# Kernel optimization log

Measured on AMD Instinct MI355X. Metric: run time of the kernel, lower is better.

The kernel has to match this reference:

```python
import jax, jax.numpy as jnp
import numpy as np

EMB = 128     # embedding_size
HEADS = 4     # n_heads
LAYERS = 2    # n_layers
T = 10        # number of graphs / timesteps (== window_size)
N = 20000     # nodes per graph
E = 320000    # edges per graph
B = 4096      # clf_nodes
WIN = 10      # window_size
NEG_SLOPE = 0.2


def setup_inputs() -> dict:
    key = jax.random.key(0)
    ks = jax.random.split(key, 26)
    p = lambda k, shape: 0.05 * jax.random.normal(k, shape, jnp.float32)
    inp = {
        "embeddings": jax.random.normal(ks[0], (T, N, EMB), jnp.float32),
        "edges": jax.random.randint(ks[1], (T, 2, E), 0, N),
        "node_type": jax.random.randint(ks[2], (T, N), 0, 4),
        "edge_type": jax.random.randint(ks[3], (T, E), 0, 4),
        "clf_neighbors": jax.random.randint(ks[4], (B,), 0, N),
        "clf_nodes": jax.random.randint(ks[5], (B,), 0, N),
        # branch 1 GAT stacks: lin weight [L, H*C, D], attention vecs [L, H, C], bias [L, H*C]
        "gat_W1": p(ks[6], (LAYERS, HEADS * EMB, EMB)),
        "gat_as1": p(ks[7], (LAYERS, HEADS, EMB)),
        "gat_ad1": p(ks[8], (LAYERS, HEADS, EMB)),
        "gat_b1": p(ks[9], (LAYERS, HEADS * EMB)),
        "lin_W1": p(ks[10], (LAYERS, EMB, HEADS * EMB)),
        "lin_b1": p(ks[11], (LAYERS, EMB)),
        # branch 2
        "gat_W2": p(ks[12], (LAYERS, HEADS * EMB, EMB)),
        "gat_as2": p(ks[13], (LAYERS, HEADS, EMB)),
        "gat_ad2": p(ks[14], (LAYERS, HEADS, EMB)),
        "gat_b2": p(ks[15], (LAYERS, HEADS * EMB)),
        "lin_W2": p(ks[16], (LAYERS, EMB, HEADS * EMB)),
        "lin_b2": p(ks[17], (LAYERS, EMB)),
        # head MLP (fc1 consumes flattened [window * 2*D])
        "fc1_W": p(ks[18], (EMB, 2 * EMB * WIN)),
        "fc1_b": p(ks[19], (EMB,)),
        "fc2_W": p(ks[20], (2, EMB)),
        "fc2_b": p(ks[21], (2,)),
    }
    return inp


def _gat(x, src, dst, W, a_s, a_d, b):
    """PyG-style GATConv (concat=True, self-loops already in src/dst, eval mode)."""
    n = x.shape[0]
    h = (x @ W.T).reshape(n, HEADS, EMB)                       # [N,H,C]
    logits = jax.nn.leaky_relu((h * a_s).sum(-1)[src] + (h * a_d).sum(-1)[dst], NEG_SLOPE)  # [Etot,H]
    logits = logits - jax.ops.segment_max(logits, dst, num_segments=n)[dst]
    ex = jnp.exp(logits)
    alpha = ex / jax.ops.segment_sum(ex, dst, num_segments=n)[dst]  # segment softmax over targets
    out = jax.ops.segment_sum(alpha[:, :, None] * h[src], dst, num_segments=n)  # [N,H,C]
    return out.reshape(n, HEADS * EMB) + b


def _branch(embeddings, edges, gW, gas, gad, gb, lW, lb):
    loops = jnp.arange(N)

    def step(carry, inputs):
        x, edge = inputs
        src = jnp.concatenate([edge[0], loops])  # add self loops (PyG default)
        dst = jnp.concatenate([edge[1], loops])
        for i in range(LAYERS):
            x = _gat(x, src, dst, gW[i], gas[i], gad[i], gb[i])
            x = jax.nn.relu(x @ lW[i].T + lb[i])
        return carry, x

    _, outs = jax.lax.scan(step, 0, (embeddings, edges))
    return outs  # [T,N,EMB]


def reference(embeddings, edges, node_type, edge_type, clf_neighbors, clf_nodes,
              gat_W1, gat_as1, gat_ad1, gat_b1, lin_W1, lin_b1,
              gat_W2, gat_as2, gat_ad2, gat_b2, lin_W2, lin_b2,
              fc1_W, fc1_b, fc2_W, fc2_b):
    o1 = _branch(embeddings, edges, gat_W1, gat_as1, gat_ad1, gat_b1, lin_W1, lin_b1)
    o2 = _branch(embeddings, edges, gat_W2, gat_as2, gat_ad2, gat_b2, lin_W2, lin_b2)
    # original prepends each graph's output -> reversed timestep order
    e1 = o1[::-1][:, clf_nodes].transpose(1, 0, 2)  # [B,T,EMB]
    e2 = o2[::-1][:, clf_nodes].transpose(1, 0, 2)
    temp = jnp.concatenate([e1, e2], axis=2)        # [B,T,2*EMB]
    # slen == window_size -> skip buffer is fully filled by temp
    flat = temp.reshape(temp.shape[0], WIN * 2 * EMB)
    h = jax.nn.relu(flat @ fc1_W.T + fc1_b)
    return jax.nn.relu(h @ fc2_W.T + fc2_b)        # [B,2]
```

## Files before the change

kernel.cpp:

```cpp
#include <hip/hip_runtime.h>
#include <cstdint>

#define NNODES 20000
#define NEDGES 320000
#define ETOT   340000
#define TSTEPS 10
#define BCLF   4096
#define EMB    128
#define HC     512
#define NEG_SLOPE 0.2f

#define NSB    64
#define SBSPAN 313
#define PCAP   6912
#define ECHUNK 2048
#define NCHUNKS ((NEDGES + ECHUNK - 1) / ECHUNK)
#define NSCHUNK ((NNODES + 255) / 256)
#define STAGECAP 7424

typedef _Float16 half_t;
typedef __attribute__((ext_vector_type(8))) _Float16 half8;
typedef __attribute__((ext_vector_type(4))) float floatx4;

__global__ void cvt_split_kernel(const float* __restrict__ in,
                                 half_t* __restrict__ hi, half_t* __restrict__ lo, long n4) {
    long i = (long)blockIdx.x * 256 + threadIdx.x;
    if (i >= n4) return;
    float4 v = *(const float4*)&in[i * 4];
    half_t h[4], l[4];
    h[0] = (half_t)v.x; l[0] = (half_t)(v.x - (float)h[0]);
    h[1] = (half_t)v.y; l[1] = (half_t)(v.y - (float)h[1]);
    h[2] = (half_t)v.z; l[2] = (half_t)(v.z - (float)h[2]);
    h[3] = (half_t)v.w; l[3] = (half_t)(v.w - (float)h[3]);
    *(unsigned long long*)&hi[i * 4] = *(unsigned long long*)h;
    *(unsigned long long*)&lo[i * 4] = *(unsigned long long*)l;
}

__global__ __launch_bounds__(256) void part64_kernel(const int* __restrict__ edges,
                                                     int* __restrict__ bcnt,
                                                     int* __restrict__ pairs) {
    int g = blockIdx.y;
    int c = blockIdx.x;
    __shared__ int hist[NSB], gbase[NSB], cur[NSB];
    if (threadIdx.x < NSB) hist[threadIdx.x] = 0;
    __syncthreads();
    const int* srcp = edges + (long)g * 2 * NEDGES;
    const int* dstp = srcp + NEDGES;
    int e0 = c * ECHUNK + threadIdx.x;
    int s[8], d[8], sb[8];
#pragma unroll
    for (int i = 0; i < 8; i++) {
        int e = e0 + i * 256;
        if (e < NEDGES) {
            s[i] = srcp[e];
            d[i] = dstp[e];
            sb[i] = (int)((unsigned)d[i] / (unsigned)SBSPAN);
            atomicAdd(&hist[sb[i]], 1);
        } else sb[i] = -1;
    }
    __syncthreads();
    if (threadIdx.x < NSB) {
        int h = hist[threadIdx.x];
        gbase[threadIdx.x] = h ? atomicAdd(&bcnt[g * NSB + threadIdx.x], h) : 0;
        cur[threadIdx.x] = 0;
    }
    __syncthreads();
#pragma unroll
    for (int i = 0; i < 8; i++) {
        if (sb[i] >= 0) {
            int pos = gbase[sb[i]] + atomicAdd(&cur[sb[i]], 1);
            int v = s[i] | ((d[i] - sb[i] * SBSPAN) << 15);
            pairs[((long)(g * NSB + sb[i])) * PCAP + pos] = v;
        }
    }
}

__global__ __launch_bounds__(256) void count_sb_kernel(const int* __restrict__ pairs,
                                                       const int* __restrict__ bcnt,
                                                       int* __restrict__ counts) {
    int g = blockIdx.x >> 6, sb = blockIdx.x & 63;
    __shared__ int hist[SBSPAN];
    for (int i = threadIdx.x; i < SBSPAN; i += 256) hist[i] = 0;
    __syncthreads();
    int n0 = sb * SBSPAN;
    int cnt = bcnt[g * NSB + sb];
    const int* p = pairs + (long)(g * NSB + sb) * PCAP;
    for (int k = threadIdx.x; k < cnt; k += 256)
        atomicAdd(&hist[p[k] >> 15], 1);
    __syncthreads();
    int nn = min(SBSPAN, NNODES - n0);
    for (int i = threadIdx.x; i < nn; i += 256)
        counts[g * NNODES + n0 + i] = hist[i];
}

__global__ void scanA_kernel(const int* __restrict__ counts, int* __restrict__ bsum) {
    int g = blockIdx.x / NSCHUNK, ch = blockIdx.x % NSCHUNK;
    int i = ch * 256 + threadIdx.x;
    int v = (i < NNODES) ? counts[g * NNODES + i] + 1 : 0;
    for (int off = 32; off; off >>= 1) v += __shfl_down(v, off);
    __shared__ int ws[4];
    if ((threadIdx.x & 63) == 0) ws[threadIdx.x >> 6] = v;
    __syncthreads();
    if (threadIdx.x == 0) bsum[blockIdx.x] = ws[0] + ws[1] + ws[2] + ws[3];
}

__global__ void scanB_kernel(const int* __restrict__ bsum, int* __restrict__ boff,
                             int* __restrict__ rowptr) {
    int g = blockIdx.x;
    int tid = threadIdx.x;
    int v = (tid < NSCHUNK) ? bsum[g * NSCHUNK + tid] : 0;
    __shared__ int buf[128];
    buf[tid] = v;
    __syncthreads();
    for (int off = 1; off < 128; off <<= 1) {
        int t = (tid >= off) ? buf[tid - off] : 0;
        __syncthreads();
        buf[tid] += t;
        __syncthreads();
    }
    if (tid < NSCHUNK) boff[g * NSCHUNK + tid] = buf[tid] - v;
    if (tid == 127) rowptr[g * (NNODES + 1) + NNODES] = buf[127];
}

__global__ void scanC_kernel(const int* __restrict__ counts, const int* __restrict__ boff,
                             int* __restrict__ rowptr) {
    int g = blockIdx.x / NSCHUNK, ch = blockIdx.x % NSCHUNK;
    int tid = threadIdx.x;
    int i = ch * 256 + tid;
    int v = (i < NNODES) ? counts[g * NNODES + i] + 1 : 0;
    __shared__ int buf[256];
    buf[tid] = v;
    __syncthreads();
    for (int off = 1; off < 256; off <<= 1) {
        int t = (tid >= off) ? buf[tid - off] : 0;
        __syncthreads();
        buf[tid] += t;
        __syncthreads();
    }
    int excl = boff[blockIdx.x] + buf[tid] - v;
    if (i < NNODES) rowptr[g * (NNODES + 1) + i] = excl;
}

__global__ __launch_bounds__(256) void fill_sb_kernel(const int* __restrict__ pairs,
                                                      const int* __restrict__ bcnt,
                                                      const int* __restrict__ rowptr,
                                                      int* __restrict__ csr_src) {
    int g = blockIdx.x >> 6, sb = blockIdx.x & 63;
    __shared__ int cur[SBSPAN];
    __shared__ int stage[STAGECAP];
    int n0 = sb * SBSPAN;
    int nn = min(SBSPAN, NNODES - n0);
    const int* rp = rowptr + g * (NNODES + 1);
    int base = rp[n0];
    int span = rp[n0 + nn] - base;
    for (int i = threadIdx.x; i < nn; i += 256) {
        int rb = rp[n0 + i] - base;
        stage[rb] = n0 + i;
        cur[i] = rb + 1;
    }
    __syncthreads();
    int cnt = bcnt[g * NSB + sb];
    const int* p = pairs + (long)(g * NSB + sb) * PCAP;
    for (int k = threadIdx.x; k < cnt; k += 256) {
        int v = p[k];
        int pos = atomicAdd(&cur[v >> 15], 1);
        stage[pos] = v & 0x7fff;
    }
    __syncthreads();
    int* dst = csr_src + (long)g * ETOT + base;
    for (int k = threadIdx.x; k < span; k += 256) dst[k] = stage[k];
}

__global__ void prep_was_kernel(const float* __restrict__ W1, const float* __restrict__ W2,
                                const float* __restrict__ as1, const float* __restrict__ as2,
                                const float* __restrict__ ad1, const float* __restrict__ ad2,
                                float* __restrict__ was, float* __restrict__ wad) {
    int b = blockIdx.x;
    int l = b >> 3, z = (b >> 2) & 1, h = b & 3;
    int k = threadIdx.x;
    const float* W  = z ? W2 : W1;
    const float* av = z ? as2 : as1;
    const float* dv = z ? ad2 : ad1;
    float s = 0.f, d = 0.f;
    for (int c = 0; c < 128; c++) {
        float w = W[(long)l * HC * EMB + (h * 128 + c) * 128 + k];
        s = fmaf(w, av[(l * 4 + h) * 128 + c], s);
        d = fmaf(w, dv[(l * 4 + h) * 128 + c], d);
    }
    long idx = ((l * 2 + z) * 4 + h) * 128 + k;
    was[idx] = s;
    wad[idx] = d;
}

__global__ void pack_ws_kernel(const float* __restrict__ wasb, const float* __restrict__ wadb,
                               half_t* __restrict__ WS0h, half_t* __restrict__ WS0l,
                               half_t* __restrict__ WS1h, half_t* __restrict__ WS1l) {
    int b = blockIdx.x;
    int k = threadIdx.x;
    if (b < 16) {
        int z = b >> 3, d = (b >> 2) & 1, h = b & 3;
        const float* src = d ? wadb : wasb;
        float v = src[((long)z * 4 + h) * 128 + k];
        half_t hi = (half_t)v;
        WS0h[b * 128 + k] = hi;
        WS0l[b * 128 + k] = (half_t)(v - (float)hi);
    } else {
        int b2 = b - 16;
        int z = b2 >> 4, r = b2 & 15;
        float v = 0.f;
        if (r < 8) {
            int d = r >> 2, h = r & 3;
            const float* src = d ? wadb : wasb;
            v = src[((long)(2 + z) * 4 + h) * 128 + k];
        }
        half_t hi = (half_t)v;
        WS1h[(z * 16 + r) * 128 + k] = hi;
        WS1l[(z * 16 + r) * 128 + k] = (half_t)(v - (float)hi);
    }
}

__global__ void prep_M_kernel(const float* __restrict__ gW1, const float* __restrict__ gW2,
                              const float* __restrict__ lW1, const float* __restrict__ lW2,
                              half_t* __restrict__ Mh, half_t* __restrict__ Ml) {
    int k = blockIdx.x;
    int inst = blockIdx.y;
    int l = inst >> 1, z = inst & 1;
    int c = threadIdx.x;
    const float* gW = (z ? gW2 : gW1) + (long)l * HC * EMB;
    const float* lW = (z ? lW2 : lW1) + (long)l * EMB * HC;
    float acc[4] = {0.f, 0.f, 0.f, 0.f};
    for (int cp = 0; cp < 128; cp++) {
#pragma unroll
        for (int h = 0; h < 4; h++) {
            float lw = lW[(long)k * 512 + h * 128 + cp];
            float gw = gW[(long)(h * 128 + cp) * 128 + c];
            acc[h] = fmaf(lw, gw, acc[h]);
        }
    }
#pragma unroll
    for (int h = 0; h < 4; h++) {
        long o = ((long)inst * 128 + k) * 512 + h * 128 + c;
        half_t hi = (half_t)acc[h];
        Mh[o] = hi;
        Ml[o] = (half_t)(acc[h] - (float)hi);
    }
}

__global__ void prep_cb_kernel(const float* __restrict__ lW1, const float* __restrict__ lW2,
                               const float* __restrict__ gb1_, const float* __restrict__ gb2_,
                               const float* __restrict__ lb1_, const float* __restrict__ lb2_,
                               float* __restrict__ cb) {
    int inst = blockIdx.x;
    int l = inst >> 1, z = inst & 1;
    int k = threadIdx.x;
    const float* lW = (z ? lW2 : lW1) + (long)l * EMB * HC;
    const float* gb = (z ? gb2_ : gb1_) + l * HC;
    const float* lb = (z ? lb2_ : lb1_) + l * EMB;
    float a = lb[k];
    for (int j = 0; j < 512; j++) a = fmaf(lW[(long)k * 512 + j], gb[j], a);
    cb[inst * 128 + k] = a;
}

__global__ __launch_bounds__(256) void scores_b(
    const half_t* __restrict__ Ahb, const half_t* __restrict__ Alb, long aInst,
    const half_t* __restrict__ WShb, const half_t* __restrict__ WSlb, long wInst, int wMask,
    float* __restrict__ outb, long oInst, int M, int OS, int CMAX) {
    int iy = blockIdx.y;
    const half_t* Ah = Ahb + (long)iy * aInst;
    const half_t* Al = Alb + (long)iy * aInst;
    const half_t* WSh = WShb + (long)(iy & wMask) * wInst;
    const half_t* WSl = WSlb + (long)(iy & wMask) * wInst;
    float* out = outb + (long)iy * oInst;
    __shared__ half_t Bh[16 * 128];
    __shared__ half_t Bl[16 * 128];
    int tid = threadIdx.x;
    *(half8*)&Bh[tid * 8] = *(const half8*)&WSh[tid * 8];
    *(half8*)&Bl[tid * 8] = *(const half8*)&WSl[tid * 8];
    __syncthreads();
    int wave = tid >> 6, lane = tid & 63;
    int l16 = lane & 15, chunk = lane >> 4;
    int r0 = blockIdx.x * 64 + wave * 16;
    int rowc = r0 + l16; if (rowc > M - 1) rowc = M - 1;
    floatx4 acc = (floatx4)0.f;
#pragma unroll
    for (int ko = 0; ko < 128; ko += 32) {
        half8 ah = *(const half8*)&Ah[(long)rowc * 128 + ko + chunk * 8];
        half8 al = *(const half8*)&Al[(long)rowc * 128 + ko + chunk * 8];
        half8 bh = *(const half8*)&Bh[l16 * 128 + ko + chunk * 8];
        half8 bl = *(const half8*)&Bl[l16 * 128 + ko + chunk * 8];
        acc = __builtin_amdgcn_mfma_f32_16x16x32_f16(ah, bh, acc, 0, 0, 0);
        acc = __builtin_amdgcn_mfma_f32_16x16x32_f16(ah, bl, acc, 0, 0, 0);
        acc = __builtin_amdgcn_mfma_f32_16x16x32_f16(al, bh, acc, 0, 0, 0);
    }
#pragma unroll
    for (int reg = 0; reg < 4; reg++) {
        int rr = r0 + chunk * 4 + reg;
        if (rr < M && l16 < CMAX) out[(long)rr * OS + l16] = acc[reg];
    }
}

template <bool SX>
__global__ __launch_bounds__(256) void agg2_kernel(
    const half_t* __restrict__ X0b, const half_t* __restrict__ X1b, long xsT,
    const float* __restrict__ sAb, const float* __restrict__ sBb, int stsh, long ssT,
    const int* __restrict__ rowptr, const int* __restrict__ csr_src,
    half_t* __restrict__ Yh, half_t* __restrict__ Yl, int t0) {
    int tz = blockIdx.y, t = t0 + tz;
    int n = blockIdx.x * 4 + (threadIdx.x >> 6);
    int lane = threadIdx.x & 63;
    int h = lane >> 4, cg = lane & 15;
    const int* rp = rowptr + t * (NNODES + 1);
    int beg = rp[n], end = rp[n + 1];
    const int* cs = csr_src + (long)t * ETOT;
    const half_t* X0 = X0b + (long)tz * xsT;
    const half_t* X1 = SX ? X0 : (X1b + (long)tz * xsT);
    const float* sA = sAb + (long)tz * ssT;
    const float* sB = sBb + (long)tz * ssT;
    float sd0 = sA[((long)n << stsh) + 4 + h];
    float sd1 = sB[((long)n << stsh) + 4 + h];
    float acc0[8], acc1[8];
#pragma unroll
    for (int c = 0; c < 8; c++) { acc0[c] = 0.f; acc1[c] = 0.f; }
    float den0 = 0.f, den1 = 0.f;

    auto proc2 = [&](int s0, int s1) {
        float va0 = sA[((long)s0 << stsh) + h];
        float vb0 = sB[((long)s0 << stsh) + h];
        float va1 = sA[((long)s1 << stsh) + h];
        float vb1 = sB[((long)s1 << stsh) + h];
        half8 xa0 = *(const half8*)&X0[(long)s0 * 128 + cg * 8];
        half8 xa1 = *(const half8*)&X0[(long)s1 * 128 + cg * 8];
        half8 xb0, xb1;
        if (!SX) {
            xb0 = *(const half8*)&X1[(long)s0 * 128 + cg * 8];
            xb1 = *(const half8*)&X1[(long)s1 * 128 + cg * 8];
        }
        float La0 = va0 + sd0, Lb0 = vb0 + sd1;
        float La1 = va1 + sd0, Lb1 = vb1 + sd1;
        float wa0 = __expf(fmaxf(La0, NEG_SLOPE * La0));
        float wb0 = __expf(fmaxf(Lb0, NEG_SLOPE * Lb0));
        float wa1 = __expf(fmaxf(La1, NEG_SLOPE * La1));
        float wb1 = __expf(fmaxf(Lb1, NEG_SLOPE * Lb1));
        den0 += wa0 + wa1;
        den1 += wb0 + wb1;
#pragma unroll
        for (int c = 0; c < 8; c++) {
            float a = acc0[c];
            a = fmaf(wa0, (float)xa0[c], a);
            a = fmaf(wa1, (float)xa1[c], a);
            acc0[c] = a;
            float b = acc1[c];
            b = fmaf(wb0, (float)(SX ? xa0[c] : xb0[c]), b);
            b = fmaf(wb1, (float)(SX ? xa1[c] : xb1[c]), b);
            acc1[c] = b;
        }
    };

    int j = beg;
    if (end - beg >= 4) {
        int a0 = cs[j], a1 = cs[j + 1];
        while (j + 4 <= end) {
            int b0 = cs[j + 2], b1 = cs[j + 3];
            proc2(a0, a1);
            a0 = b0; a1 = b1;
            j += 2;
        }
        proc2(a0, a1);
        j += 2;
    }
    for (; j < end; j++) {
        int src = cs[j];
        float va = sA[((long)src << stsh) + h];
        float vb = sB[((long)src << stsh) + h];
        half8 xa = *(const half8*)&X0[(long)src * 128 + cg * 8];
        half8 xb;
        if (!SX) xb = *(const half8*)&X1[(long)src * 128 + cg * 8];
        float La = va + sd0, Lb = vb + sd1;
        float wa = __expf(fmaxf(La, NEG_SLOPE * La));
        float wb = __expf(fmaxf(Lb, NEG_SLOPE * Lb));
        den0 += wa;
        den1 += wb;
#pragma unroll
        for (int c = 0; c < 8; c++) {
            acc0[c] = fmaf(wa, (float)xa[c], acc0[c]);
            acc1[c] = fmaf(wb, (float)(SX ? xa[c] : xb[c]), acc1[c]);
        }
    }

    float inv0 = 1.0f / den0;
    float inv1 = 1.0f / den1;
    half8 oh0, ol0, oh1, ol1;
#pragma unroll
    for (int c = 0; c < 8; c++) {
        float v0 = acc0[c] * inv0;
        half_t h0 = (half_t)v0;
        oh0[c] = h0; ol0[c] = (half_t)(v0 - (float)h0);
        float v1 = acc1[c] * inv1;
        half_t h1 = (half_t)v1;
        oh1[c] = h1; ol1[c] = (half_t)(v1 - (float)h1);
    }
    long yb0 = ((long)(tz * 2) * NNODES + n) * 512 + h * 128 + cg * 8;
    long yb1 = yb0 + (long)NNODES * 512;
    *(half8*)&Yh[yb0] = oh0;
    *(half8*)&Yl[yb0] = ol0;
    *(half8*)&Yh[yb1] = oh1;
    *(half8*)&Yl[yb1] = ol1;
}

__global__ __launch_bounds__(256) void gemm_b(
    const half_t* __restrict__ Ahb, const half_t* __restrict__ Alb, long aInst,
    const half_t* __restrict__ Bhb, const half_t* __restrict__ Blb, long bInst,
    const float* __restrict__ biasb, long biasInst,
    half_t* __restrict__ Ch, half_t* __restrict__ Cl,
    long cInst, int M, int N, int K) {
    const int i = blockIdx.z;
    const half_t* __restrict__ Ah = Ahb + (long)i * aInst;
    const half_t* __restrict__ Al = Alb + (long)i * aInst;
    const half_t* __restrict__ Bh = Bhb + (long)(i & 1) * bInst;
    const half_t* __restrict__ Bl = Blb + (long)(i & 1) * bInst;
    const float* __restrict__ bias = biasb + (long)(i & 1) * biasInst;

    __shared__ half_t Ash[4 * 128 * 8];
    __shared__ half_t Asl[4 * 128 * 8];
    __shared__ half_t Bsh[4 * 128 * 8];
    __shared__ half_t Bsl[4 * 128 * 8];

    const int tid = threadIdx.x;
    const int row0 = blockIdx.x * 128;
    const int col0 = blockIdx.y * 128;
    const int wave = tid >> 6;
    const int lane = tid & 63;
    const int wm = (wave >> 1) * 64;
    const int wn = (wave & 1) * 64;
    const int chunk = lane >> 4;
    const int l16 = lane & 15;

    floatx4 acc[4][4];
#pragma unroll
    for (int ii = 0; ii < 4; ii++)
#pragma unroll
        for (int j = 0; j < 4; j++) acc[ii][j] = (floatx4)0.0f;

    for (int k0 = 0; k0 < K; k0 += 32) {
        __syncthreads();
#pragma unroll
        for (int p = 0; p < 2; p++) {
            int idx = p * 256 + tid;
            int r = idx >> 2, kc = idx & 3;
            int arow = row0 + r;
            half8 vah, val;
            if (arow < M) {
                vah = *(const half8*)&Ah[(long)arow * K + k0 + kc * 8];
                val = *(const half8*)&Al[(long)arow * K + k0 + kc * 8];
            } else {
#pragma unroll
                for (int q = 0; q < 8; q++) { vah[q] = (half_t)0.f; val[q] = (half_t)0.f; }
            }
            *(half8*)&Ash[(kc * 128 + r) * 8] = vah;
            *(half8*)&Asl[(kc * 128 + r) * 8] = val;
            long boff = (long)(col0 + r) * K + k0 + kc * 8;
            *(half8*)&Bsh[(kc * 128 + r) * 8] = *(const half8*)&Bh[boff];
            *(half8*)&Bsl[(kc * 128 + r) * 8] = *(const half8*)&Bl[boff];
        }
        __syncthreads();
        half8 afh[4], afl[4], bfh[4], bfl[4];
#pragma unroll
        for (int mi = 0; mi < 4; mi++) {
            int o = (chunk * 128 + wm + mi * 16 + l16) * 8;
            afh[mi] = *(const half8*)&Ash[o];
            afl[mi] = *(const half8*)&Asl[o];
        }
#pragma unroll
        for (int ni = 0; ni < 4; ni++) {
            int o = (chunk * 128 + wn + ni * 16 + l16) * 8;
            bfh[ni] = *(const half8*)&Bsh[o];
            bfl[ni] = *(const half8*)&Bsl[o];
        }
#pragma unroll
        for (int mi = 0; mi < 4; mi++)
#pragma unroll
            for (int ni = 0; ni < 4; ni++) {
                acc[mi][ni] = __builtin_amdgcn_mfma_f32_16x16x32_f16(
                    afh[mi], bfh[ni], acc[mi][ni], 0, 0, 0);
                acc[mi][ni] = __builtin_amdgcn_mfma_f32_16x16x32_f16(
                    afh[mi], bfl[ni], acc[mi][ni], 0, 0, 0);
                acc[mi][ni] = __builtin_amdgcn_mfma_f32_16x16x32_f16(
                    afl[mi], bfh[ni], acc[mi][ni], 0, 0, 0);
            }
    }

    const int r4 = (lane >> 4) * 4;
#pragma unroll
    for (int mi = 0; mi < 4; mi++) {
#pragma unroll
        for (int reg = 0; reg < 4; reg++) {
            int row = row0 + wm + mi * 16 + r4 + reg;
            if (row >= M) continue;
#pragma unroll
            for (int ni = 0; ni < 4; ni++) {
                int col = col0 + wn + ni * 16 + l16;
                float v = fmaxf(acc[mi][ni][reg] + bias[col], 0.f);
                long o = (long)i * cInst + (long)row * N + col;
                half_t hi = (half_t)v;
                Ch[o] = hi;
                Cl[o] = (half_t)(v - (float)hi);
            }
        }
    }
}

__global__ __launch_bounds__(256) void fc1_part_kernel(
    const half_t* __restrict__ Ah, const half_t* __restrict__ Al,
    const half_t* __restrict__ Bh, const half_t* __restrict__ Bl,
    float* __restrict__ pbuf, int M, int N, int K, int kslice) {
    const int ks = blockIdx.y;
    const int kbeg = ks * kslice;
    const int kend = kbeg + kslice;

    __shared__ half_t Ash[4 * 128 * 8];
    __shared__ half_t Asl[4 * 128 * 8];
    __shared__ half_t Bsh[4 * 128 * 8];
    __shared__ half_t Bsl[4 * 128 * 8];

    const int tid = threadIdx.x;
    const int row0 = blockIdx.x * 128;
    const int wave = tid >> 6;
    const int lane = tid & 63;
    const int wm = (wave >> 1) * 64;
    const int wn = (wave & 1) * 64;
    const int chunk = lane >> 4;
    const int l16 = lane & 15;

    floatx4 acc[4][4];
#pragma unroll
    for (int ii = 0; ii < 4; ii++)
#pragma unroll
        for (int j = 0; j < 4; j++) acc[ii][j] = (floatx4)0.0f;

    for (int k0 = kbeg; k0 < kend; k0 += 32) {
        __syncthreads();
#pragma unroll
        for (int p = 0; p < 2; p++) {
            int idx = p * 256 + tid;
            int r = idx >> 2, kc = idx & 3;
            long aoff = (long)(row0 + r) * K + k0 + kc * 8;
            *(half8*)&Ash[(kc * 128 + r) * 8] = *(const half8*)&Ah[aoff];
            *(half8*)&Asl[(kc * 128 + r) * 8] = *(const half8*)&Al[aoff];
            long boff = (long)r * K + k0 + kc * 8;
            *(half8*)&Bsh[(kc * 128 + r) * 8] = *(const half8*)&Bh[boff];
            *(half8*)&Bsl[(kc * 128 + r) * 8] = *(const half8*)&Bl[boff];
        }
        __syncthreads();
        half8 afh[4], afl[4], bfh[4], bfl[4];
#pragma unroll
        for (int mi = 0; mi < 4; mi++) {
            int o = (chunk * 128 + wm + mi * 16 + l16) * 8;
            afh[mi] = *(const half8*)&Ash[o];
            afl[mi] = *(const half8*)&Asl[o];
        }
#pragma unroll
        for (int ni = 0; ni < 4; ni++) {
            int o = (chunk * 128 + wn + ni * 16 + l16) * 8;
            bfh[ni] = *(const half8*)&Bsh[o];
            bfl[ni] = *(const half8*)&Bsl[o];
        }
#pragma unroll
        for (int mi = 0; mi < 4; mi++)
#pragma unroll
            for (int ni = 0; ni < 4; ni++) {
                acc[mi][ni] = __builtin_amdgcn_mfma_f32_16x16x32_f16(
                    afh[mi], bfh[ni], acc[mi][ni], 0, 0, 0);
                acc[mi][ni] = __builtin_amdgcn_mfma_f32_16x16x32_f16(
                    afh[mi], bfl[ni], acc[mi][ni], 0, 0, 0);
                acc[mi][ni] = __builtin_amdgcn_mfma_f32_16x16x32_f16(
                    afl[mi], bfh[ni], acc[mi][ni], 0, 0, 0);
            }
    }

    const int r4 = (lane >> 4) * 4;
#pragma unroll
    for (int mi = 0; mi < 4; mi++)
#pragma unroll
        for (int reg = 0; reg < 4; reg++) {
            int row = row0 + wm + mi * 16 + r4 + reg;
#pragma unroll
            for (int ni = 0; ni < 4; ni++) {
                int col = wn + ni * 16 + l16;
                pbuf[((long)ks * M + row) * N + col] = acc[mi][ni][reg];
            }
        }
}

__global__ void fc1_reduce_kernel(const float* __restrict__ pbuf, const float* __restrict__ bias,
                                  float* __restrict__ h1, int MN, int KS) {
    int i = blockIdx.x * 256 + threadIdx.x;
    if (i >= MN) return;
    float a = 0.f;
    for (int ks = 0; ks < KS; ks++) a += pbuf[(long)ks * MN + i];
    h1[i] = fmaxf(a + bias[i & (EMB - 1)], 0.f);
}

__global__ void gather_kernel(const half_t* __restrict__ Xh, const half_t* __restrict__ Xl,
                              const int* __restrict__ clf,
                              half_t* __restrict__ flath, half_t* __restrict__ flatl, int t0) {
    int b = blockIdx.x;
    int z = blockIdx.y;
    int tz = blockIdx.z;
    int t = t0 + tz, gz = tz * 2 + z;
    int j = threadIdx.x;
    int node = clf[b];
    long dst = (long)b * (TSTEPS * 2 * EMB) + (TSTEPS - 1 - t) * (2 * EMB) + z * EMB;
    long src = ((long)gz * NNODES + node) * EMB;
    ((unsigned int*)&flath[dst])[j] = ((const unsigned int*)&Xh[src])[j];
    ((unsigned int*)&flatl[dst])[j] = ((const unsigned int*)&Xl[src])[j];
}

__global__ void fc2_kernel(const float* __restrict__ h1, const float* __restrict__ W,
                           const float* __restrict__ bias, float* __restrict__ out) {
    int row = blockIdx.x;
    int lane = threadIdx.x;
    float x0 = h1[(long)row * 128 + lane];
    float x1 = h1[(long)row * 128 + 64 + lane];
    float p0 = x0 * W[lane] + x1 * W[64 + lane];
    float p1 = x0 * W[128 + lane] + x1 * W[192 + lane];
    for (int off = 32; off; off >>= 1) {
        p0 += __shfl_down(p0, off);
        p1 += __shfl_down(p1, off);
    }
    if (lane == 0) {
        out[row * 2 + 0] = fmaxf(p0 + bias[0], 0.f);
        out[row * 2 + 1] = fmaxf(p1 + bias[1], 0.f);
    }
}

extern "C" void kernel_launch(void* const* d_in, const int* in_sizes, int n_in,
                              void* d_out, int out_size, void* d_ws, size_t ws_size,
                              hipStream_t stream) {
    const float* emb     = (const float*)d_in[0];
    const int*   edges   = (const int*)d_in[1];
    const int*   clf     = (const int*)d_in[5];
    const float* gat_W1  = (const float*)d_in[6];
    const float* gat_as1 = (const float*)d_in[7];
    const float* gat_ad1 = (const float*)d_in[8];
    const float* gat_b1  = (const float*)d_in[9];
    const float* lin_W1  = (const float*)d_in[10];
    const float* lin_b1  = (const float*)d_in[11];
    const float* gat_W2  = (const float*)d_in[12];
    const float* gat_as2 = (const float*)d_in[13];
    const float* gat_ad2 = (const float*)d_in[14];
    const float* gat_b2  = (const float*)d_in[15];
    const float* lin_W2  = (const float*)d_in[16];
    const float* lin_b2  = (const float*)d_in[17];
    const float* fc1_W   = (const float*)d_in[18];
    const float* fc1_b   = (const float*)d_in[19];
    const float* fc2_W   = (const float*)d_in[20];
    const float* fc2_b   = (const float*)d_in[21];
    float* out = (float*)d_out;

    char* ws = (char*)d_ws;
    size_t off = 0;
    auto alloc = [&](size_t bytes) -> char* {
        char* p = ws + off;
        off += (bytes + 255) & ~(size_t)255;
        return p;
    };
    int* counts  = (int*)alloc((size_t)TSTEPS * NNODES * 4);
    int* rowptr  = (int*)alloc((size_t)TSTEPS * (NNODES + 1) * 4);
    int* csr_src = (int*)alloc((size_t)TSTEPS * ETOT * 4);
    int* bsum    = (int*)alloc((size_t)TSTEPS * NSCHUNK * 4);
    int* boff    = (int*)alloc((size_t)TSTEPS * NSCHUNK * 4);
    int* bcnt    = (int*)alloc((size_t)TSTEPS * NSB * 4);
    half_t* embh = (half_t*)alloc((size_t)TSTEPS * NNODES * EMB * 2);
    half_t* Mh   = (half_t*)alloc((size_t)4 * EMB * HC * 2);
    half_t* Ml   = (half_t*)alloc((size_t)4 * EMB * HC * 2);
    float*  cb   = (float*)alloc((size_t)4 * EMB * 4);
    half_t* fc1Wh = (half_t*)alloc((size_t)EMB * 2 * EMB * TSTEPS * 2);
    half_t* fc1Wl = (half_t*)alloc((size_t)EMB * 2 * EMB * TSTEPS * 2);
    float* wasb = (float*)alloc((size_t)2 * 2 * 4 * 128 * 4);
    float* wadb = (float*)alloc((size_t)2 * 2 * 4 * 128 * 4);
    half_t* WS0h = (half_t*)alloc((size_t)16 * 128 * 2);
    half_t* WS0l = (half_t*)alloc((size_t)16 * 128 * 2);
    half_t* WS1h = (half_t*)alloc((size_t)2 * 16 * 128 * 2);
    half_t* WS1l = (half_t*)alloc((size_t)2 * 16 * 128 * 2);
    float* s0buf = (float*)alloc((size_t)TSTEPS * NNODES * 16 * 4);
    half_t* flath = (half_t*)alloc((size_t)BCLF * (TSTEPS * 2 * EMB) * 2);
    half_t* flatl = (half_t*)alloc((size_t)BCLF * (TSTEPS * 2 * EMB) * 2);
    float* h1buf = (float*)alloc((size_t)BCLF * EMB * 4);

    size_t region_base = off;
    half_t* embl = (half_t*)alloc((size_t)TSTEPS * NNODES * EMB * 2);
    int* pairs   = (int*)alloc((size_t)TSTEPS * NSB * PCAP * 4);

    const size_t perT = ((size_t)2 * NNODES * HC * 2 * 2) +
                        ((size_t)2 * NNODES * EMB * 2 * 2) +
                        ((size_t)2 * NNODES * 8 * 4) + 2048;
    int TG = 1;
    if (ws_size > region_base + perT) {
        size_t cap = (ws_size - region_base) / perT;
        TG = (cap >= 10) ? 10 : (int)cap;
        if (TG < 1) TG = 1;
    }
    off = region_base;
    half_t* Yh = (half_t*)alloc((size_t)TG * 2 * NNODES * HC * 2);
    half_t* Yl = (half_t*)alloc((size_t)TG * 2 * NNODES * HC * 2);
    half_t* Xh = (half_t*)alloc((size_t)TG * 2 * NNODES * EMB * 2);
    half_t* Xl = (half_t*)alloc((size_t)TG * 2 * NNODES * EMB * 2);
    float* s1buf = (float*)alloc((size_t)TG * 2 * NNODES * 8 * 4);

    {
        long n4 = (long)TSTEPS * NNODES * EMB / 4;
        cvt_split_kernel<<<(int)((n4 + 255) / 256), 256, 0, stream>>>(emb, embh, embl, n4);
        long f4 = (long)EMB * 2 * EMB * TSTEPS / 4;
        cvt_split_kernel<<<(int)((f4 + 255) / 256), 256, 0, stream>>>(fc1_W, fc1Wh, fc1Wl, f4);
    }
    prep_was_kernel<<<16, 128, 0, stream>>>(gat_W1, gat_W2, gat_as1, gat_as2,
                                            gat_ad1, gat_ad2, wasb, wadb);
    pack_ws_kernel<<<48, 128, 0, stream>>>(wasb, wadb, WS0h, WS0l, WS1h, WS1l);
    prep_M_kernel<<<dim3(128, 4), 128, 0, stream>>>(gat_W1, gat_W2, lin_W1, lin_W2, Mh, Ml);
    prep_cb_kernel<<<4, 128, 0, stream>>>(lin_W1, lin_W2, gat_b1, gat_b2, lin_b1, lin_b2, cb);

    scores_b<<<dim3(3125, 1), 256, 0, stream>>>(
        embh, embl, 0, WS0h, WS0l, 0, 0, s0buf, 0, TSTEPS * NNODES, 16, 16);

    hipMemsetAsync(bcnt, 0, (size_t)TSTEPS * NSB * 4, stream);
    part64_kernel<<<dim3(NCHUNKS, TSTEPS), 256, 0, stream>>>(edges, bcnt, pairs);
    count_sb_kernel<<<NSB * TSTEPS, 256, 0, stream>>>(pairs, bcnt, counts);
    scanA_kernel<<<TSTEPS * NSCHUNK, 256, 0, stream>>>(counts, bsum);
    scanB_kernel<<<TSTEPS, 128, 0, stream>>>(bsum, boff, rowptr);
    scanC_kernel<<<TSTEPS * NSCHUNK, 256, 0, stream>>>(counts, boff, rowptr);
    fill_sb_kernel<<<NSB * TSTEPS, 256, 0, stream>>>(pairs, bcnt, rowptr, csr_src);

    for (int t0 = 0; t0 < TSTEPS; t0 += TG) {
        int tg = (TSTEPS - t0 < TG) ? (TSTEPS - t0) : TG;
        agg2_kernel<true><<<dim3(5000, tg), 256, 0, stream>>>(
            embh + (long)t0 * NNODES * EMB, nullptr, (long)NNODES * EMB,
            s0buf + (long)t0 * NNODES * 16, s0buf + (long)t0 * NNODES * 16 + 8,
            4, (long)NNODES * 16,
            rowptr, csr_src, Yh, Yl, t0);
        gemm_b<<<dim3(157, 1, 2 * tg), 256, 0, stream>>>(
            Yh, Yl, (long)NNODES * HC,
            Mh, Ml, (long)EMB * HC, cb, EMB,
            Xh, Xl, (long)NNODES * EMB, NNODES, EMB, HC);
        scores_b<<<dim3(313, 2 * tg), 256, 0, stream>>>(
            Xh, Xl, (long)NNODES * EMB,
            WS1h, WS1l, (long)16 * 128, 1,
            s1buf, (long)NNODES * 8, NNODES, 8, 8);
        agg2_kernel<false><<<dim3(5000, tg), 256, 0, stream>>>(
            Xh, Xh + (long)NNODES * EMB, (long)2 * NNODES * EMB,
            s1buf, s1buf + (long)NNODES * 8, 3, (long)2 * NNODES * 8,
            rowptr, csr_src, Yh, Yl, t0);
        gemm_b<<<dim3(157, 1, 2 * tg), 256, 0, stream>>>(
            Yh, Yl, (long)NNODES * HC,
            Mh + (long)2 * EMB * HC, Ml + (long)2 * EMB * HC, (long)EMB * HC,
            cb + 2 * EMB, EMB,
            Xh, Xl, (long)NNODES * EMB, NNODES, EMB, HC);
        gather_kernel<<<dim3(BCLF, 2, tg), 64, 0, stream>>>(Xh, Xl, clf, flath, flatl, t0);
    }
    float* pbuf = (float*)Yh;
    fc1_part_kernel<<<dim3(32, 8), 256, 0, stream>>>(
        flath, flatl, fc1Wh, fc1Wl, pbuf, BCLF, EMB, TSTEPS * 2 * EMB, (TSTEPS * 2 * EMB) / 8);
    fc1_reduce_kernel<<<(BCLF * EMB + 255) / 256, 256, 0, stream>>>(
        pbuf, fc1_b, h1buf, BCLF * EMB, 8);
    fc2_kernel<<<BCLF, 64, 0, stream>>>(h1buf, fc2_W, fc2_b, out);
}
```

Before: 1.723 ms.

## Fuse GAT aggregation with per-node projection GEMM through shared memory

Merges the edge aggregation kernel and the following projection GEMM into one kernel. Each 1024-thread block aggregates 16 nodes for both branches, keeps the 512-wide split-half results in swizzled LDS, and then runs MFMA against the combined weight matrix to write the 128-wide output with bias and ReLU. This removes the global write and re-read of the large intermediate Y buffers and two kernel launches per layer, and shrinks the workspace. In exchange the weights are read straight from global memory by every block without LDS tiling, and the bigger blocks with their LDS use may limit occupancy. The second layer now writes to a separate output buffer so it does not overwrite its own input.

New measurement: 2.451 ms. 42.3% more time.

```diff
diff --git a/kernel.cpp b/kernel.cpp
--- a/kernel.cpp
+++ b/kernel.cpp
@@ -300,211 +300,153 @@
 }
 
 template <bool SX>
-__global__ __launch_bounds__(256) void agg2_kernel(
+__global__ __launch_bounds__(1024, 8) void aggproj_kernel(
     const half_t* __restrict__ X0b, const half_t* __restrict__ X1b, long xsT,
     const float* __restrict__ sAb, const float* __restrict__ sBb, int stsh, long ssT,
     const int* __restrict__ rowptr, const int* __restrict__ csr_src,
-    half_t* __restrict__ Yh, half_t* __restrict__ Yl, int t0) {
+    const half_t* __restrict__ Mh_l, const half_t* __restrict__ Ml_l,
+    const float* __restrict__ cb_l,
+    half_t* __restrict__ Xouth, half_t* __restrict__ Xoutl, int t0) {
+    __shared__ half_t Yh_lds[2 * 16 * 512];
+    __shared__ half_t Yl_lds[2 * 16 * 512];
+
     int tz = blockIdx.y, t = t0 + tz;
-    int n = blockIdx.x * 4 + (threadIdx.x >> 6);
+    int n0 = blockIdx.x * 16;
+    int w = threadIdx.x >> 6;
     int lane = threadIdx.x & 63;
     int h = lane >> 4, cg = lane & 15;
-    const int* rp = rowptr + t * (NNODES + 1);
-    int beg = rp[n], end = rp[n + 1];
-    const int* cs = csr_src + (long)t * ETOT;
-    const half_t* X0 = X0b + (long)tz * xsT;
-    const half_t* X1 = SX ? X0 : (X1b + (long)tz * xsT);
-    const float* sA = sAb + (long)tz * ssT;
-    const float* sB = sBb + (long)tz * ssT;
-    float sd0 = sA[((long)n << stsh) + 4 + h];
-    float sd1 = sB[((long)n << stsh) + 4 + h];
-    float acc0[8], acc1[8];
-#pragma unroll
-    for (int c = 0; c < 8; c++) { acc0[c] = 0.f; acc1[c] = 0.f; }
-    float den0 = 0.f, den1 = 0.f;
-
-    auto proc2 = [&](int s0, int s1) {
-        float va0 = sA[((long)s0 << stsh) + h];
-        float vb0 = sB[((long)s0 << stsh) + h];
-        float va1 = sA[((long)s1 << stsh) + h];
-        float vb1 = sB[((long)s1 << stsh) + h];
-        half8 xa0 = *(const half8*)&X0[(long)s0 * 128 + cg * 8];
-        half8 xa1 = *(const half8*)&X0[(long)s1 * 128 + cg * 8];
-        half8 xb0, xb1;
-        if (!SX) {
-            xb0 = *(const half8*)&X1[(long)s0 * 128 + cg * 8];
-            xb1 = *(const half8*)&X1[(long)s1 * 128 + cg * 8];
-        }
-        float La0 = va0 + sd0, Lb0 = vb0 + sd1;
-        float La1 = va1 + sd0, Lb1 = vb1 + sd1;
-        float wa0 = __expf(fmaxf(La0, NEG_SLOPE * La0));
-        float wb0 = __expf(fmaxf(Lb0, NEG_SLOPE * Lb0));
-        float wa1 = __expf(fmaxf(La1, NEG_SLOPE * La1));
-        float wb1 = __expf(fmaxf(Lb1, NEG_SLOPE * Lb1));
-        den0 += wa0 + wa1;
-        den1 += wb0 + wb1;
+
+    {
+        int n = n0 + w;
+        const int* rp = rowptr + t * (NNODES + 1);
+        int beg = rp[n], end = rp[n + 1];
+        const int* cs = csr_src + (long)t * ETOT;
+        const half_t* X0 = X0b + (long)tz * xsT;
+        const half_t* X1 = SX ? X0 : (X1b + (long)tz * xsT);
+        const float* sA = sAb + (long)tz * ssT;
+        const float* sB = sBb + (long)tz * ssT;
+        float sd0 = sA[((long)n << stsh) + 4 + h];
+        float sd1 = sB[((long)n << stsh) + 4 + h];
+        float acc0[8], acc1[8];
+#pragma unroll
+        for (int c = 0; c < 8; c++) { acc0[c] = 0.f; acc1[c] = 0.f; }
+        float den0 = 0.f, den1 = 0.f;
+
+        auto proc2 = [&](int s0, int s1) {
+            float va0 = sA[((long)s0 << stsh) + h];
+            float vb0 = sB[((long)s0 << stsh) + h];
+            float va1 = sA[((long)s1 << stsh) + h];
+            float vb1 = sB[((long)s1 << stsh) + h];
+            half8 xa0 = *(const half8*)&X0[(long)s0 * 128 + cg * 8];
+            half8 xa1 = *(const half8*)&X0[(long)s1 * 128 + cg * 8];
+            half8 xb0, xb1;
+            if (!SX) {
+                xb0 = *(const half8*)&X1[(long)s0 * 128 + cg * 8];
+                xb1 = *(const half8*)&X1[(long)s1 * 128 + cg * 8];
+            }
+            float La0 = va0 + sd0, Lb0 = vb0 + sd1;
+            float La1 = va1 + sd0, Lb1 = vb1 + sd1;
+            float wa0 = __expf(fmaxf(La0, NEG_SLOPE * La0));
+            float wb0 = __expf(fmaxf(Lb0, NEG_SLOPE * Lb0));
+            float wa1 = __expf(fmaxf(La1, NEG_SLOPE * La1));
+            float wb1 = __expf(fmaxf(Lb1, NEG_SLOPE * Lb1));
+            den0 += wa0 + wa1;
+            den1 += wb0 + wb1;
+#pragma unroll
+            for (int c = 0; c < 8; c++) {
+                float a = acc0[c];
+                a = fmaf(wa0, (float)xa0[c], a);
+                a = fmaf(wa1, (float)xa1[c], a);
+                acc0[c] = a;
+                float b = acc1[c];
+                b = fmaf(wb0, (float)(SX ? xa0[c] : xb0[c]), b);
+                b = fmaf(wb1, (float)(SX ? xa1[c] : xb1[c]), b);
+                acc1[c] = b;
+            }
+        };
+
+        int j = beg;
+        if (end - beg >= 4) {
+            int a0 = cs[j], a1 = cs[j + 1];
+            while (j + 4 <= end) {
+                int b0 = cs[j + 2], b1 = cs[j + 3];
+                proc2(a0, a1);
+                a0 = b0; a1 = b1;
+                j += 2;
+            }
+            proc2(a0, a1);
+            j += 2;
+        }
+        for (; j < end; j++) {
+            int src = cs[j];
+            float va = sA[((long)src << stsh) + h];
+            float vb = sB[((long)src << stsh) + h];
+            half8 xa = *(const half8*)&X0[(long)src * 128 + cg * 8];
+            half8 xb;
+            if (!SX) xb = *(const half8*)&X1[(long)src * 128 + cg * 8];
+            float La = va + sd0, Lb = vb + sd1;
+            float wa = __expf(fmaxf(La, NEG_SLOPE * La));
+            float wb = __expf(fmaxf(Lb, NEG_SLOPE * Lb));
+            den0 += wa;
+            den1 += wb;
+#pragma unroll
+            for (int c = 0; c < 8; c++) {
+                acc0[c] = fmaf(wa, (float)xa[c], acc0[c]);
+                acc1[c] = fmaf(wb, (float)(SX ? xa[c] : xb[c]), acc1[c]);
+            }
+        }
+
+        float inv0 = 1.0f / den0;
+        float inv1 = 1.0f / den1;
+        half8 oh0, ol0, oh1, ol1;
 #pragma unroll
         for (int c = 0; c < 8; c++) {
-            float a = acc0[c];
-            a = fmaf(wa0, (float)xa0[c], a);
-            a = fmaf(wa1, (float)xa1[c], a);
-            acc0[c] = a;
-            float b = acc1[c];
-            b = fmaf(wb0, (float)(SX ? xa0[c] : xb0[c]), b);
-            b = fmaf(wb1, (float)(SX ? xa1[c] : xb1[c]), b);
-            acc1[c] = b;
-        }
-    };
-
-    int j = beg;
-    if (end - beg >= 4) {
-        int a0 = cs[j], a1 = cs[j + 1];
-        while (j + 4 <= end) {
-            int b0 = cs[j + 2], b1 = cs[j + 3];
-            proc2(a0, a1);
-            a0 = b0; a1 = b1;
-            j += 2;
-        }
-        proc2(a0, a1);
-        j += 2;
-    }
-    for (; j < end; j++) {
-        int src = cs[j];
-        float va = sA[((long)src << stsh) + h];
-        float vb = sB[((long)src << stsh) + h];
-        half8 xa = *(const half8*)&X0[(long)src * 128 + cg * 8];
-        half8 xb;
-        if (!SX) xb = *(const half8*)&X1[(long)src * 128 + cg * 8];
-        float La = va + sd0, Lb = vb + sd1;
-        float wa = __expf(fmaxf(La, NEG_SLOPE * La));
-        float wb = __expf(fmaxf(Lb, NEG_SLOPE * Lb));
-        den0 += wa;
-        den1 += wb;
-#pragma unroll
-        for (int c = 0; c < 8; c++) {
-            acc0[c] = fmaf(wa, (float)xa[c], acc0[c]);
-            acc1[c] = fmaf(wb, (float)(SX ? xa[c] : xb[c]), acc1[c]);
-        }
-    }
-
-    float inv0 = 1.0f / den0;
-    float inv1 = 1.0f / den1;
-    half8 oh0, ol0, oh1, ol1;
-#pragma unroll
-    for (int c = 0; c < 8; c++) {
-        float v0 = acc0[c] * inv0;
-        half_t h0 = (half_t)v0;
-        oh0[c] = h0; ol0[c] = (half_t)(v0 - (float)h0);
-        float v1 = acc1[c] * inv1;
-        half_t h1 = (half_t)v1;
-        oh1[c] = h1; ol1[c] = (half_t)(v1 - (float)h1);
-    }
-    long yb0 = ((long)(tz * 2) * NNODES + n) * 512 + h * 128 + cg * 8;
-    long yb1 = yb0 + (long)NNODES * 512;
-    *(half8*)&Yh[yb0] = oh0;
-    *(half8*)&Yl[yb0] = ol0;
-    *(half8*)&Yh[yb1] = oh1;
-    *(half8*)&Yl[yb1] = ol1;
-}
-
-__global__ __launch_bounds__(256) void gemm_b(
-    const half_t* __restrict__ Ahb, const half_t* __restrict__ Alb, long aInst,
-    const half_t* __restrict__ Bhb, const half_t* __restrict__ Blb, long bInst,
-    const float* __restrict__ biasb, long biasInst,
-    half_t* __restrict__ Ch, half_t* __restrict__ Cl,
-    long cInst, int M, int N, int K) {
-    const int i = blockIdx.z;
-    const half_t* __restrict__ Ah = Ahb + (long)i * aInst;
-    const half_t* __restrict__ Al = Alb + (long)i * aInst;
-    const half_t* __restrict__ Bh = Bhb + (long)(i & 1) * bInst;
-    const half_t* __restrict__ Bl = Blb + (long)(i & 1) * bInst;
-    const float* __restrict__ bias = biasb + (long)(i & 1) * biasInst;
-
-    __shared__ half_t Ash[4 * 128 * 8];
-    __shared__ half_t Asl[4 * 128 * 8];
-    __shared__ half_t Bsh[4 * 128 * 8];
-    __shared__ half_t Bsl[4 * 128 * 8];
-
-    const int tid = threadIdx.x;
-    const int row0 = blockIdx.x * 128;
-    const int col0 = blockIdx.y * 128;
-    const int wave = tid >> 6;
-    const int lane = tid & 63;
-    const int wm = (wave >> 1) * 64;
-    const int wn = (wave & 1) * 64;
-    const int chunk = lane >> 4;
-    const int l16 = lane & 15;
-
-    floatx4 acc[4][4];
-#pragma unroll
-    for (int ii = 0; ii < 4; ii++)
-#pragma unroll
-        for (int j = 0; j < 4; j++) acc[ii][j] = (floatx4)0.0f;
-
-    for (int k0 = 0; k0 < K; k0 += 32) {
-        __syncthreads();
-#pragma unroll
-        for (int p = 0; p < 2; p++) {
-            int idx = p * 256 + tid;
-            int r = idx >> 2, kc = idx & 3;
-            int arow = row0 + r;
-            half8 vah, val;
-            if (arow < M) {
-                vah = *(const half8*)&Ah[(long)arow * K + k0 + kc * 8];
-                val = *(const half8*)&Al[(long)arow * K + k0 + kc * 8];
-            } else {
-#pragma unroll
-                for (int q = 0; q < 8; q++) { vah[q] = (half_t)0.f; val[q] = (half_t)0.f; }
-            }
-            *(half8*)&Ash[(kc * 128 + r) * 8] = vah;
-            *(half8*)&Asl[(kc * 128 + r) * 8] = val;
-            long boff = (long)(col0 + r) * K + k0 + kc * 8;
-            *(half8*)&Bsh[(kc * 128 + r) * 8] = *(const half8*)&Bh[boff];
-            *(half8*)&Bsl[(kc * 128 + r) * 8] = *(const half8*)&Bl[boff];
-        }
-        __syncthreads();
-        half8 afh[4], afl[4], bfh[4], bfl[4];
-#pragma unroll
-        for (int mi = 0; mi < 4; mi++) {
-            int o = (chunk * 128 + wm + mi * 16 + l16) * 8;
-            afh[mi] = *(const half8*)&Ash[o];
-            afl[mi] = *(const half8*)&Asl[o];
-        }
-#pragma unroll
-        for (int ni = 0; ni < 4; ni++) {
-            int o = (chunk * 128 + wn + ni * 16 + l16) * 8;
-            bfh[ni] = *(const half8*)&Bsh[o];
-            bfl[ni] = *(const half8*)&Bsl[o];
-        }
-#pragma unroll
-        for (int mi = 0; mi < 4; mi++)
-#pragma unroll
-            for (int ni = 0; ni < 4; ni++) {
-                acc[mi][ni] = __builtin_amdgcn_mfma_f32_16x16x32_f16(
-                    afh[mi], bfh[ni], acc[mi][ni], 0, 0, 0);
-                acc[mi][ni] = __builtin_amdgcn_mfma_f32_16x16x32_f16(
-                    afh[mi], bfl[ni], acc[mi][ni], 0, 0, 0);
-                acc[mi][ni] = __builtin_amdgcn_mfma_f32_16x16x32_f16(
-                    afl[mi], bfh[ni], acc[mi][ni], 0, 0, 0);
-            }
-    }
-
-    const int r4 = (lane >> 4) * 4;
-#pragma unroll
-    for (int mi = 0; mi < 4; mi++) {
+            float v0 = acc0[c] * inv0;
+            half_t h0 = (half_t)v0;
+            oh0[c] = h0; ol0[c] = (half_t)(v0 - (float)h0);
+            float v1 = acc1[c] * inv1;
+            half_t h1 = (half_t)v1;
+            oh1[c] = h1; ol1[c] = (half_t)(v1 - (float)h1);
+        }
+        int Gp = (h * 16 + cg) ^ (w & 7);
+        *(half8*)&Yh_lds[((0 * 16 + w) * 64 + Gp) * 8] = oh0;
+        *(half8*)&Yl_lds[((0 * 16 + w) * 64 + Gp) * 8] = ol0;
+        *(half8*)&Yh_lds[((1 * 16 + w) * 64 + Gp) * 8] = oh1;
+        *(half8*)&Yl_lds[((1 * 16 + w) * 64 + Gp) * 8] = ol1;
+    }
+    __syncthreads();
+
+    {
+        int z2 = w >> 3, jt = w & 7;
+        const half_t* __restrict__ Bh = Mh_l + (long)z2 * EMB * HC;
+        const half_t* __restrict__ Bl = Ml_l + (long)z2 * EMB * HC;
+        const float* __restrict__ bias = cb_l + z2 * EMB;
+        int l16 = lane & 15, chunk = lane >> 4;
+        floatx4 acc = (floatx4)0.f;
+#pragma unroll
+        for (int kc = 0; kc < 16; kc++) {
+            int Gp = (kc * 4 + chunk) ^ (l16 & 7);
+            half8 ah = *(const half8*)&Yh_lds[((z2 * 16 + l16) * 64 + Gp) * 8];
+            half8 al = *(const half8*)&Yl_lds[((z2 * 16 + l16) * 64 + Gp) * 8];
+            long bo = (long)(jt * 16 + l16) * HC + kc * 32 + chunk * 8;
+            half8 bh = *(const half8*)&Bh[bo];
+            half8 bl = *(const half8*)&Bl[bo];
+            acc = __builtin_amdgcn_mfma_f32_16x16x32_f16(ah, bh, acc, 0, 0, 0);
+            acc = __builtin_amdgcn_mfma_f32_16x16x32_f16(ah, bl, acc, 0, 0, 0);
+            acc = __builtin_amdgcn_mfma_f32_16x16x32_f16(al, bh, acc, 0, 0, 0);
+        }
+        int r4 = (lane >> 4) * 4;
+        long gz = (long)tz * 2 + z2;
+        int col = jt * 16 + l16;
+        float bv = bias[col];
 #pragma unroll
         for (int reg = 0; reg < 4; reg++) {
-            int row = row0 + wm + mi * 16 + r4 + reg;
-            if (row >= M) continue;
-#pragma unroll
-            for (int ni = 0; ni < 4; ni++) {
-                int col = col0 + wn + ni * 16 + l16;
-                float v = fmaxf(acc[mi][ni][reg] + bias[col], 0.f);
-                long o = (long)i * cInst + (long)row * N + col;
-                half_t hi = (half_t)v;
-                Ch[o] = hi;
-                Cl[o] = (half_t)(v - (float)hi);
-            }
+            int row = r4 + reg;
+            float v = fmaxf(acc[reg] + bv, 0.f);
+            long o = (gz * NNODES + n0 + row) * EMB + col;
+            half_t hi = (half_t)v;
+            Xouth[o] = hi;
+            Xoutl[o] = (half_t)(v - (float)hi);
         }
     }
 }
@@ -691,9 +633,8 @@
     half_t* embl = (half_t*)alloc((size_t)TSTEPS * NNODES * EMB * 2);
     int* pairs   = (int*)alloc((size_t)TSTEPS * NSB * PCAP * 4);
 
-    const size_t perT = ((size_t)2 * NNODES * HC * 2 * 2) +
-                        ((size_t)2 * NNODES * EMB * 2 * 2) +
-                        ((size_t)2 * NNODES * 8 * 4) + 2048;
+    const size_t perT = ((size_t)2 * NNODES * EMB * 2 * 2) * 2 +
+                        ((size_t)2 * NNODES * 8 * 4) + 4096;
     int TG = 1;
     if (ws_size > region_base + perT) {
         size_t cap = (ws_size - region_base) / perT;
@@ -701,10 +642,10 @@
         if (TG < 1) TG = 1;
     }
     off = region_base;
-    half_t* Yh = (half_t*)alloc((size_t)TG * 2 * NNODES * HC * 2);
-    half_t* Yl = (half_t*)alloc((size_t)TG * 2 * NNODES * HC * 2);
-    half_t* Xh = (half_t*)alloc((size_t)TG * 2 * NNODES * EMB * 2);
-    half_t* Xl = (half_t*)alloc((size_t)TG * 2 * NNODES * EMB * 2);
+    half_t* Xh  = (half_t*)alloc((size_t)TG * 2 * NNODES * EMB * 2);
+    half_t* Xl  = (half_t*)alloc((size_t)TG * 2 * NNODES * EMB * 2);
+    half_t* X2h = (half_t*)alloc((size_t)TG * 2 * NNODES * EMB * 2);
+    half_t* X2l = (half_t*)alloc((size_t)TG * 2 * NNODES * EMB * 2);
     float* s1buf = (float*)alloc((size_t)TG * 2 * NNODES * 8 * 4);
 
     {
@@ -732,31 +673,26 @@
 
     for (int t0 = 0; t0 < TSTEPS; t0 += TG) {
         int tg = (TSTEPS - t0 < TG) ? (TSTEPS - t0) : TG;
-        agg2_kernel<true><<<dim3(5000, tg), 256, 0, stream>>>(
+        aggproj_kernel<true><<<dim3(NNODES / 16, tg), 1024, 0, stream>>>(
             embh + (long)t0 * NNODES * EMB, nullptr, (long)NNODES * EMB,
             s0buf + (long)t0 * NNODES * 16, s0buf + (long)t0 * NNODES * 16 + 8,
             4, (long)NNODES * 16,
-            rowptr, csr_src, Yh, Yl, t0);
-        gemm_b<<<dim3(157, 1, 2 * tg), 256, 0, stream>>>(
-            Yh, Yl, (long)NNODES * HC,
-            Mh, Ml, (long)EMB * HC, cb, EMB,
-            Xh, Xl, (long)NNODES * EMB, NNODES, EMB, HC);
+            rowptr, csr_src,
+            Mh, Ml, cb,
+            Xh, Xl, t0);
         scores_b<<<dim3(313, 2 * tg), 256, 0, stream>>>(
             Xh, Xl, (long)NNODES * EMB,
             WS1h, WS1l, (long)16 * 128, 1,
             s1buf, (long)NNODES * 8, NNODES, 8, 8);
-        agg2_kernel<false><<<dim3(5000, tg), 256, 0, stream>>>(
+        aggproj_kernel<false><<<dim3(NNODES / 16, tg), 1024, 0, stream>>>(
             Xh, Xh + (long)NNODES * EMB, (long)2 * NNODES * EMB,
             s1buf, s1buf + (long)NNODES * 8, 3, (long)2 * NNODES * 8,
-            rowptr, csr_src, Yh, Yl, t0);
-        gemm_b<<<dim3(157, 1, 2 * tg), 256, 0, stream>>>(
-            Yh, Yl, (long)NNODES * HC,
-            Mh + (long)2 * EMB * HC, Ml + (long)2 * EMB * HC, (long)EMB * HC,
-            cb + 2 * EMB, EMB,
-            Xh, Xl, (long)NNODES * EMB, NNODES, EMB, HC);
-        gather_kernel<<<dim3(BCLF, 2, tg), 64, 0, stream>>>(Xh, Xl, clf, flath, flatl, t0);
-    }
-    float* pbuf = (float*)Yh;
+            rowptr, csr_src,
+            Mh + (long)2 * EMB * HC, Ml + (long)2 * EMB * HC, cb + 2 * EMB,
+            X2h, X2l, t0);
+        gather_kernel<<<dim3(BCLF, 2, tg), 64, 0, stream>>>(X2h, X2l, clf, flath, flatl, t0);
+    }
+    float* pbuf = (float*)(ws + region_base);
     fc1_part_kernel<<<dim3(32, 8), 256, 0, stream>>>(
         flath, flatl, fc1Wh, fc1Wl, pbuf, BCLF, EMB, TSTEPS * 2 * EMB, (TSTEPS * 2 * EMB) / 8);
     fc1_reduce_kernel<<<(BCLF * EMB + 255) / 256, 256, 0, stream>>>(
```
